# Performance work log

Hardware: AMD Instinct MI355X
Metric: run time of the kernel (lower is better)

The kernel has to match this reference:

```python
import jax, jax.numpy as jnp
import numpy as np
from jax import lax

PRE_NMS_THRESH = 0.05
PRE_NMS_TOP_N = 1000
FINAL_NMS_THRESH = 0.4  # hardcoded in forward(): boxlist_nms(..., 0.4)
MIN_SIZE = 0
STRIDE = 4.0
NEG = -1e9

N, C, H, W = 32, 1, 384, 384


def setup_inputs() -> dict:
    key = jax.random.key(0)
    k1, k2 = jax.random.split(key)
    box_cls = jax.random.uniform(k1, (N, C, H, W), dtype=jnp.float32)
    box_regression = jax.random.normal(k2, (N, 4, H, W), dtype=jnp.float32) * 20.0
    image_sizes = jnp.full((N, 2), H * int(STRIDE), dtype=jnp.int32)
    return {"box_cls": box_cls, "box_regression": box_regression, "image_sizes": image_sizes}


def decode_boxes(quad):
    # quad: [N, 4, H, W]; EAST geometry decode at stride 4 -> xyxy
    n, _, h, w = quad.shape
    x = (jnp.arange(w, dtype=quad.dtype) * STRIDE)[None, :]   # [1, W]
    y = (jnp.arange(h, dtype=quad.dtype) * STRIDE)[:, None]   # [H, 1]
    ymin = y - quad[:, 0]
    xmax = x + quad[:, 1]
    ymax = y + quad[:, 2]
    xmin = x - quad[:, 3]
    return jnp.stack([xmin, ymin, xmax, ymax], axis=1)  # [N, 4, H, W] (permute (3,0,1,2))


def iou_matrix(b):
    # b: [K, 4] xyxy
    x1, y1, x2, y2 = b[:, 0], b[:, 1], b[:, 2], b[:, 3]
    area = jnp.clip(x2 - x1, 0) * jnp.clip(y2 - y1, 0)
    ix1 = jnp.maximum(x1[:, None], x1[None, :])
    iy1 = jnp.maximum(y1[:, None], y1[None, :])
    ix2 = jnp.minimum(x2[:, None], x2[None, :])
    iy2 = jnp.minimum(y2[:, None], y2[None, :])
    inter = jnp.clip(ix2 - ix1, 0) * jnp.clip(iy2 - iy1, 0)
    union = area[:, None] + area[None, :] - inter
    return inter / jnp.maximum(union, 1e-9)


def greedy_nms(boxes, init_keep):
    # boxes: [K, 4] sorted by descending score; init_keep: [K] bool
    K = boxes.shape[0]
    iou = iou_matrix(boxes)
    idx = jnp.arange(K)

    def body(i, keep):
        suppress = (iou[i] > FINAL_NMS_THRESH) & (idx > i)
        return jnp.where(keep[i], keep & ~suppress, keep)

    return lax.fori_loop(0, K, body, init_keep)


def _forward(box_cls, box_regression):
    n, c, h, w = box_cls.shape
    boxes = decode_boxes(box_regression)                       # [N, 4, H, W]
    boxes = boxes.transpose(0, 2, 3, 1).reshape(n, h * w, 4)   # [N, HW, 4]
    scores = box_cls.transpose(0, 2, 3, 1).reshape(n, h * w)   # [N, HW] (C=1)

    # threshold + conditional top-k (padding with NEG emulates variable counts)
    masked = jnp.where(scores > PRE_NMS_THRESH, scores, NEG)
    scores_k, idx_k = lax.top_k(masked, PRE_NMS_TOP_N)         # [N, K], sorted desc
    boxes_k = jnp.take_along_axis(boxes, idx_k[..., None], axis=1)  # [N, K, 4]

    valid = scores_k > PRE_NMS_THRESH
    ws = boxes_k[..., 2] - boxes_k[..., 0]
    hs = boxes_k[..., 3] - boxes_k[..., 1]
    valid = valid & (ws >= MIN_SIZE) & (hs >= MIN_SIZE)        # remove_small_boxes

    keep = jax.vmap(greedy_nms)(boxes_k, valid)                # [N, K]
    out = jnp.concatenate([boxes_k, scores_k[..., None]], axis=-1)
    out = out * keep[..., None].astype(out.dtype)              # [N, K, 5]
    return out, keep


def reference(box_cls, box_regression, image_sizes):
    return _forward(box_cls, box_regression)
```

## Files before the change

kernel.cpp:

```cpp
#include <hip/hip_runtime.h>
#include <stdint.h>

#define NIMG 32
#define WID 384
#define HW 147456
#define TOPK 1000
#define KPAD 1024
#define NBINS 512
#define BIN_SCALEF 512.0f
#define SEGCAP 128
#define CANDCAP 2048
#define THRESH 0.05f
#define PREF_C 0.99f
#define NMS_T 0.4f
#define NBLK 18
#define FINEBINS 256

typedef unsigned long long u64;
typedef unsigned int u32;

#define PIMG_OFF 0
#define PCAND_OFF 4096
#define PBOX_OFF 528384

__device__ __forceinline__ float area_of(float x0, float y0, float x1, float y1) {
  float a = fmaxf(x1 - x0, 0.0f) * fmaxf(y1 - y0, 0.0f);
  asm volatile("" : "+v"(a));
  return a;
}

__device__ __forceinline__ bool iou_gt(float ax0, float ay0, float ax1, float ay1, float aa,
                                       float bx0, float by0, float bx1, float by1, float ba) {
  float ix1 = fmaxf(ax0, bx0);
  float iy1 = fmaxf(ay0, by0);
  float ix2 = fminf(ax1, bx1);
  float iy2 = fminf(ay1, by1);
  float iw = fmaxf(ix2 - ix1, 0.0f);
  float ih = fmaxf(iy2 - iy1, 0.0f);
  float inter = iw * ih;
  asm volatile("" : "+v"(inter));
  float uni = fmaxf(aa + ba - inter, 1e-9f);
  return (inter / uni) > NMS_T;
}

__device__ __forceinline__ u64 shflxor64(u64 v, int m) {
  int lo = __shfl_xor((int)(u32)v, m, 64);
  int hi = __shfl_xor((int)(u32)(v >> 32), m, 64);
  return ((u64)(u32)hi << 32) | (u32)lo;
}

__device__ __forceinline__ u64 make_key(float s, u32 idx) {
  u32 ord = __float_as_uint(s) | 0x80000000u;
  return ((u64)ord << 32) | (u32)(~idx);
}

__device__ __forceinline__ float score_of(u64 key) {
  return __uint_as_float((u32)(key >> 32) & 0x7FFFFFFFu);
}

__device__ __forceinline__ int bin_of(float s) {
  int b = (int)(s * BIN_SCALEF);
  return b < 0 ? 0 : (b > NBINS - 1 ? NBINS - 1 : b);
}

__device__ __forceinline__ int finebin(u64 key) {
  float s = score_of(key);
  int b = (int)((s - 0.99f) * 25600.0f);
  return b < 0 ? 0 : (b > FINEBINS - 1 ? FINEBINS - 1 : b);
}

__global__ __launch_bounds__(256) void scan_kernel(const float* __restrict__ cls,
                                                   const float* __restrict__ reg,
                                                   u32* __restrict__ pimgcnt,
                                                   u64* __restrict__ pcand,
                                                   float4* __restrict__ pbox) {
  __shared__ u64 lbuf[SEGCAP];
  __shared__ u32 lcnt, sbase;
  const int n = blockIdx.y;
  const int tid = threadIdx.x;
  const int lane = tid & 63;
  if (tid == 0) lcnt = 0;
  __syncthreads();

  const float4* src = (const float4*)(cls + (size_t)n * HW) + blockIdx.x * 2048;
  float4 A[8];
#pragma unroll
  for (int v = 0; v < 8; v++) A[v] = src[tid + v * 256];

  const u64 ltmask = (1ull << lane) - 1ull;
#pragma unroll
  for (int v = 0; v < 8; v++) {
    float ss[4] = {A[v].x, A[v].y, A[v].z, A[v].w};
#pragma unroll
    for (int c = 0; c < 4; c++) {
      float s = ss[c];
      bool pc = s > PREF_C;
      u64 m = __ballot(pc);
      if (m) {
        int ldr = __ffsll(m) - 1;
        u32 wb = 0;
        if (lane == ldr) wb = atomicAdd(&lcnt, (u32)__popcll(m));
        wb = (u32)__shfl((int)wb, ldr, 64);
        if (pc) {
          u32 pos = wb + (u32)__popcll(m & ltmask);
          if (pos < SEGCAP) lbuf[pos] = make_key(s, (u32)((blockIdx.x * 2048 + tid + v * 256) * 4 + c));
        }
      }
    }
  }
  __syncthreads();
  const u32 total = lcnt;
  const u32 c = total < SEGCAP ? total : (u32)SEGCAP;
  if (tid == 0) {
    u32 add = (total > SEGCAP) ? (c + 0x100000u) : c;
    sbase = atomicAdd(&pimgcnt[n], add);
  }
  __syncthreads();
  const u32 base = sbase;
  const float* rb = reg + (size_t)n * 4 * HW;
  u64* pk = pcand + (size_t)n * CANDCAP;
  float4* pb = pbox + (size_t)n * CANDCAP;
  for (u32 i = tid; i < c; i += 256) {
    u32 slot = base + i;
    if (slot < CANDCAP) {
      u64 key = lbuf[i];
      u32 idx = ~(u32)(key & 0xFFFFFFFFull);
      int iy = (int)idx / WID;
      int ix = (int)idx - iy * WID;
      float xx = (float)ix * 4.0f;
      float yy = (float)iy * 4.0f;
      float r0 = rb[idx];
      float r1 = rb[HW + idx];
      float r2 = rb[2 * HW + idx];
      float r3 = rb[3 * HW + idx];
      float4 box;
      box.y = yy - r0; box.z = xx + r1; box.w = yy + r2; box.x = xx - r3;
      pk[slot] = key;
      pb[slot] = box;
    }
  }
}

#define REGCHAIN(K, JSTART) do {                                            \
    const bool desc_ = ((tid & ((K) >> 1)) == 0);                           \
    for (int j_ = (JSTART); j_ >= 2; j_ >>= 1) {                            \
      int h_ = j_ >> 1;                                                     \
      bool low_ = (tid & h_) == 0;                                          \
      u64 p0_ = shflxor64(e0, h_), p1_ = shflxor64(e1, h_);                 \
      bool tm_ = (low_ == desc_);                                           \
      e0 = tm_ ? (e0 > p0_ ? e0 : p0_) : (e0 < p0_ ? e0 : p0_);             \
      e1 = tm_ ? (e1 > p1_ ? e1 : p1_) : (e1 < p1_ ? e1 : p1_);             \
    }                                                                       \
    { u64 lo_ = e0 < e1 ? e0 : e1, hi_ = e0 < e1 ? e1 : e0;                 \
      e0 = desc_ ? hi_ : lo_; e1 = desc_ ? lo_ : hi_; }                     \
  } while (0)

__global__ __launch_bounds__(1024) void fused_kernel(const float* __restrict__ cls,
                                                     const float* __restrict__ reg,
                                                     const u32* __restrict__ pimgcnt,
                                                     const u64* __restrict__ pcand,
                                                     const float4* __restrict__ pbox,
                                                     float* __restrict__ out) {
  __shared__ __align__(16) unsigned char smem[90112];
  u64*    CKEY   = (u64*)smem;
  float4* CBOX   = (float4*)(smem + 16384);
  u32*    BINNED = (u32*)(smem + 49152);
  u64*    RKEY   = (u64*)(smem + 57344);
  float4* RBOX   = (float4*)(smem + 65536);
  float* vx    = (float*)smem;
  float* vy    = (float*)(smem + 4096);
  float* vz    = (float*)(smem + 8192);
  float* vw    = (float*)(smem + 12288);
  float* varea = (float*)(smem + 16384);
  u64*   mlds  = (u64*)(smem + 20480);

  __shared__ u32 BINSTART[FINEBINS + 1];
  __shared__ u32 HIST[FINEBINS];
  __shared__ u32 bs[NBINS];
  __shared__ u32 stmp[64];
  __shared__ int stbin;
  __shared__ u32 sflag, sfc;
  __shared__ int sC;
  __shared__ u32 wcnt[16], woff[16];
  __shared__ int pc[136], pk[136];
  __shared__ int sV, snch, snp;
  __shared__ u64 keepsh[16], srem[16];

  const int n = blockIdx.x;
  const int tid = threadIdx.x;
  const int lane = tid & 63;
  const int w = tid >> 6;
  const u64 ltmask = (1ull << lane) - 1ull;

  const u64* gk = pcand + (size_t)n * CANDCAP;
  const float4* gb = pbox + (size_t)n * CANDCAP;
  u64 k0 = gk[tid];
  u64 k1 = gk[tid + 1024];
  float4 b0 = gb[tid];
  float4 b1 = gb[tid + 1024];

  RKEY[tid] = 0ull;
  if (tid < FINEBINS) HIST[tid] = 0;
  if (tid == 0) {
    u32 C = pimgcnt[n];
    sC = (int)C;
    sflag = (C < TOPK || C > CANDCAP) ? 1u : 0u;
    sfc = 0;
  }
  __syncthreads();

  u64 key; float4 b;

  if (sflag == 0) {
    const int C = sC;
    if (tid < C)        { CKEY[tid] = k0;        CBOX[tid] = b0;        atomicAdd(&HIST[finebin(k0)], 1u); }
    if (tid + 1024 < C) { CKEY[tid + 1024] = k1; CBOX[tid + 1024] = b1; atomicAdd(&HIST[finebin(k1)], 1u); }
    __syncthreads();
    if (tid < 64) {
      u32 h0 = HIST[lane * 4 + 0], h1 = HIST[lane * 4 + 1];
      u32 h2 = HIST[lane * 4 + 2], h3 = HIST[lane * 4 + 3];
      u32 t = h0 + h1 + h2 + h3;
      u32 incl = t;
#pragma unroll
      for (int d = 1; d < 64; d <<= 1) {
        u32 v = (u32)__shfl_up((int)incl, d, 64);
        if (lane >= d) incl += v;
      }
      u32 base = incl - t;
      BINSTART[lane * 4 + 0] = base;
      BINSTART[lane * 4 + 1] = base + h0;
      BINSTART[lane * 4 + 2] = base + h0 + h1;
      BINSTART[lane * 4 + 3] = base + h0 + h1 + h2;
      if (lane == 63) BINSTART[FINEBINS] = incl;
      HIST[lane * 4 + 0] = 0; HIST[lane * 4 + 1] = 0;
      HIST[lane * 4 + 2] = 0; HIST[lane * 4 + 3] = 0;
    }
    __syncthreads();
    if (tid < C) {
      int bb = finebin(k0);
      u32 slot = atomicAdd(&HIST[bb], 1u);
      BINNED[BINSTART[bb] + slot] = (u32)tid;
    }
    if (tid + 1024 < C) {
      int bb = finebin(k1);
      u32 slot = atomicAdd(&HIST[bb], 1u);
      BINNED[BINSTART[bb] + slot] = (u32)(tid + 1024);
    }
    __syncthreads();
    if (tid < C) {
      u64 k = k0;
      int bb = finebin(k);
      u32 s0 = BINSTART[bb], s1 = BINSTART[bb + 1];
      u32 g = 0;
      for (u32 j = s0; j < s1; j++) { if (CKEY[BINNED[j]] > k) g++; }
      u32 rank = (u32)C - s1 + g;
      if (rank < KPAD) { RKEY[rank] = k; RBOX[rank] = b0; }
    }
    if (tid + 1024 < C) {
      u64 k = k1;
      int bb = finebin(k);
      u32 s0 = BINSTART[bb], s1 = BINSTART[bb + 1];
      u32 g = 0;
      for (u32 j = s0; j < s1; j++) { if (CKEY[BINNED[j]] > k) g++; }
      u32 rank = (u32)C - s1 + g;
      if (rank < KPAD) { RKEY[rank] = k; RBOX[rank] = b1; }
    }
    __syncthreads();
    key = RKEY[tid];
    b = (key != 0ull) ? RBOX[tid] : make_float4(0.f, 0.f, 0.f, 0.f);
  } else {
    for (int i = tid; i < NBINS; i += 1024) bs[i] = 0;
    CKEY[tid] = 0ull; CKEY[tid + 1024] = 0ull;
    __syncthreads();
    const float* ci = cls + (size_t)n * HW;
    for (int base = 0; base < HW; base += 1024) {
      float s = ci[base + tid];
      if (s > THRESH) atomicAdd(&bs[bin_of(s)], 1u);
    }
    __syncthreads();
    if (tid < 64) {
      u32 cs = 0;
#pragma unroll
      for (int k2 = 0; k2 < 8; k2++) cs += bs[lane * 8 + k2];
      u32 s = cs;
#pragma unroll
      for (int d = 1; d < 64; d <<= 1) {
        u32 v = (u32)__shfl_down((int)s, d, 64);
        if (lane + d < 64) s += v;
      }
      stmp[lane] = s;
      u64 mask = __ballot(s >= TOPK);
      if (lane == 0) {
        int t = 0;
        if (mask) {
          int L = 63 - __clzll(mask);
          u32 acc = (L < 63) ? stmp[L + 1] : 0;
          for (int bb = L * 8 + 7; bb >= L * 8; bb--) {
            acc += bs[bb];
            if (acc >= TOPK) { t = bb; break; }
          }
        }
        stbin = t;
      }
    }
    __syncthreads();
    const int t = stbin;
    for (int base = 0; base < HW; base += 1024) {
      int i = base + tid;
      float s = ci[i];
      bool p = (s > THRESH) && (bin_of(s) >= t);
      u64 m = __ballot(p);
      if (m) {
        int ldr = __ffsll(m) - 1;
        u32 wb = 0;
        if (lane == ldr) wb = atomicAdd(&sfc, (u32)__popcll(m));
        wb = (u32)__shfl((int)wb, ldr, 64);
        if (p) { u32 pos = wb + (u32)__popcll(m & ltmask); if (pos < CANDCAP) CKEY[pos] = make_key(s, (u32)i); }
      }
    }
    __syncthreads();
    {
      u64 e0 = CKEY[2 * tid], e1 = CKEY[2 * tid + 1];
      REGCHAIN(2, 1); REGCHAIN(4, 2); REGCHAIN(8, 4); REGCHAIN(16, 8);
      REGCHAIN(32, 16); REGCHAIN(64, 32); REGCHAIN(128, 64);
      for (int k = 256; k <= CANDCAP; k <<= 1) {
        CKEY[2 * tid] = e0; CKEY[2 * tid + 1] = e1;
        __syncthreads();
        for (int j = k >> 1; j >= 128; j >>= 1) {
          int i = ((tid & ~(j - 1)) << 1) | (tid & (j - 1));
          u64 a = CKEY[i], bb = CKEY[i + j];
          bool desc = ((i & k) == 0);
          if (desc ? (a < bb) : (a > bb)) { CKEY[i] = bb; CKEY[i + j] = a; }
          __syncthreads();
        }
        e0 = CKEY[2 * tid]; e1 = CKEY[2 * tid + 1];
        REGCHAIN(k, 64);
      }
      CKEY[2 * tid] = e0; CKEY[2 * tid + 1] = e1;
      __syncthreads();
    }
    key = CKEY[tid];
    b = make_float4(0.f, 0.f, 0.f, 0.f);
    if (key != 0ull && tid < TOPK) {
      u32 idx = ~(u32)(key & 0xFFFFFFFFull);
      int iy = (int)idx / WID;
      int ix = (int)idx - iy * WID;
      float xx = (float)ix * 4.0f;
      float yy = (float)iy * 4.0f;
      const float* rb = reg + (size_t)n * 4 * HW;
      float r0 = rb[idx];
      float r1 = rb[HW + idx];
      float r2 = rb[2 * HW + idx];
      float r3 = rb[3 * HW + idx];
      b.y = yy - r0; b.z = xx + r1; b.w = yy + r2; b.x = xx - r3;
    }
  }
  float s = score_of(key);
  __syncthreads();

  bool vb = (tid < TOPK) && (s > THRESH) && (b.z - b.x >= 0.0f) && (b.w - b.y >= 0.0f);
  vx[tid] = 0.0f; vy[tid] = 0.0f; vz[tid] = 0.0f; vw[tid] = 0.0f;
  varea[tid] = 0.0f;
  u64 vm = __ballot(vb);
  if (lane == 0) wcnt[w] = (u32)__popcll(vm);
  if (tid < 16) { srem[tid] = 0ull; keepsh[tid] = 0ull; }
  __syncthreads();
  if (tid < 64) {
    u32 v = (lane < 16) ? wcnt[lane] : 0u;
    u32 incl = v;
#pragma unroll
    for (int d = 1; d < 16; d <<= 1) {
      u32 t = (u32)__shfl_up((int)incl, d, 64);
      if (lane >= d) incl += t;
    }
    if (lane < 16) woff[lane] = incl - v;
    if (lane == 15) {
      int V = (int)incl;
      int nch = (V + 63) >> 6;
      sV = V; snch = nch; snp = nch * (nch + 1) / 2;
    }
  }
  __syncthreads();
  const int V = sV, nch = snch, npairs = snp;

  int pos = -1;
  if (vb) {
    pos = (int)(woff[w] + (u32)__popcll(vm & ltmask));
    vx[pos] = b.x; vy[pos] = b.y; vz[pos] = b.z; vw[pos] = b.w;
    varea[pos] = area_of(b.x, b.y, b.z, b.w);
  }
  if (tid < npairs) {
    int p = tid, c = 0, base = 0;
    while (p >= base + (nch - c)) { base += nch - c; c++; }
    pc[tid] = c; pk[tid] = c + (p - base);
  }
  __syncthreads();

  {
    int prevc = -1;
    float cx0 = 0.f, cy0 = 0.f, cx1 = 0.f, cy1 = 0.f, ca = 0.f;
    for (int r = w; r < npairs * 64; r += 16) {
      int p = r >> 6, i = r & 63;
      int c = pc[p], k = pk[p];
      if (c != prevc) {
        int ci = c * 64 + lane;
        cx0 = vx[ci]; cy0 = vy[ci]; cx1 = vz[ci]; cy1 = vw[ci]; ca = varea[ci];
        prevc = c;
      }
      int ri = k * 64 + i;
      float rx0 = vx[ri], ry0 = vy[ri], rx1 = vz[ri], ry1 = vw[ri], ra = varea[ri];
      bool pred = iou_gt(rx0, ry0, rx1, ry1, ra, cx0, cy0, cx1, cy1, ca);
      u64 m = __ballot(pred);
      if (lane == 0) mlds[r] = m;
    }
  }
  __syncthreads();

  if (tid < 64) {
    for (int c = 0; c < nch; c++) {
      int pbase = c * nch - (c * (c - 1)) / 2 - c;
      u64 diag = mlds[(pbase + c) * 64 + lane];
      u64 ainit = (V >= (c + 1) * 64) ? ~0ull
                : ((V > c * 64) ? ((1ull << (V - c * 64)) - 1ull) : 0ull);
      u64 alive;
      {
        u64 a = ainit & ~srem[c];
        u32 alo2 = __builtin_amdgcn_readfirstlane((u32)a);
        u32 ahi2 = __builtin_amdgcn_readfirstlane((u32)(a >> 32));
        alive = ((u64)ahi2 << 32) | alo2;
      }
      u32 rlo = (u32)diag, rhi = (u32)(diag >> 32);
      u64 cur = alive;
      while (cur) {
        int i = __ffsll(cur) - 1;
        u32 rl = __builtin_amdgcn_readlane(rlo, i);
        u32 rh = __builtin_amdgcn_readlane(rhi, i);
        u64 rowi = ((u64)rh << 32) | rl;
        u64 lowmask = (i == 63) ? ~0ull : ((1ull << (i + 1)) - 1ull);
        rowi &= ~lowmask;
        alive &= ~rowi;
        cur &= ~rowi;
        cur &= cur - 1;
      }
      if (lane == 0) keepsh[c] = alive;
      const u64 K = alive;
      for (int k = c + 1; k < nch; k++) {
        bool sup = (mlds[(pbase + k) * 64 + lane] & K) != 0ull;
        u64 mres = __ballot(sup);
        if (lane == 0) srem[k] |= mres;
      }
    }
  }
  __syncthreads();

  u64 kb = (vb && pos >= 0) ? ((keepsh[pos >> 6] >> (pos & 63)) & 1ull) : 0ull;
  if (tid < TOPK) {
    float f = (float)kb;
    size_t ob = (size_t)n * (TOPK * 5) + (size_t)tid * 5;
    out[ob + 0] = kb ? b.x : 0.0f;
    out[ob + 1] = kb ? b.y : 0.0f;
    out[ob + 2] = kb ? b.z : 0.0f;
    out[ob + 3] = kb ? b.w : 0.0f;
    out[ob + 4] = kb ? s : 0.0f;
    out[(size_t)NIMG * TOPK * 5 + (size_t)n * TOPK + tid] = f;
  }
}

extern "C" void kernel_launch(void* const* d_in, const int* in_sizes, int n_in,
                              void* d_out, int out_size, void* d_ws, size_t ws_size,
                              hipStream_t stream) {
  const float* cls = (const float*)d_in[0];
  const float* reg = (const float*)d_in[1];
  float* out = (float*)d_out;

  uint8_t* ws = (uint8_t*)d_ws;
  u32* pimgcnt = (u32*)(ws + PIMG_OFF);
  u64* pcand = (u64*)(ws + PCAND_OFF);
  float4* pbox = (float4*)(ws + PBOX_OFF);

  hipMemsetAsync(pimgcnt, 0, NIMG * sizeof(u32), stream);
  scan_kernel<<<dim3(NBLK, NIMG), 256, 0, stream>>>(cls, reg, pimgcnt, pcand, pbox);
  fused_kernel<<<NIMG, 1024, 0, stream>>>(cls, reg, pimgcnt, pcand, pbox, out);
}
```

Before: 157.1 us.

## Replace global atomic compaction with per-segment candidate slots and in-kernel prefix

Each scan block now writes its candidates into a fixed per-segment region and records its own count, instead of reserving space through a global atomic counter per image. The fused kernel computes a prefix sum over the 18 segment counts with wave shuffles and compacts the candidates into shared memory. This removes the hipMemsetAsync launch and the global atomic serialization, at the cost of reading 2304 slots per image instead of 2048. The shared CBOX staging buffer is also dropped, since boxes now stay in registers.

```diff
diff --git a/kernel.cpp b/kernel.cpp
--- a/kernel.cpp
+++ b/kernel.cpp
@@ -9,6 +9,7 @@
 #define NBINS 512
 #define BIN_SCALEF 512.0f
 #define SEGCAP 128
+#define NSLOT (NBLK * SEGCAP)
 #define CANDCAP 2048
 #define THRESH 0.05f
 #define PREF_C 0.99f
@@ -19,9 +20,9 @@
 typedef unsigned long long u64;
 typedef unsigned int u32;
 
-#define PIMG_OFF 0
+#define PCNT_OFF 0
 #define PCAND_OFF 4096
-#define PBOX_OFF 528384
+#define PBOX_OFF  593920
 
 __device__ __forceinline__ float area_of(float x0, float y0, float x1, float y1) {
   float a = fmaxf(x1 - x0, 0.0f) * fmaxf(y1 - y0, 0.0f);
@@ -71,11 +72,11 @@
 
 __global__ __launch_bounds__(256) void scan_kernel(const float* __restrict__ cls,
                                                    const float* __restrict__ reg,
-                                                   u32* __restrict__ pimgcnt,
+                                                   u32* __restrict__ pcnt,
                                                    u64* __restrict__ pcand,
                                                    float4* __restrict__ pbox) {
   __shared__ u64 lbuf[SEGCAP];
-  __shared__ u32 lcnt, sbase;
+  __shared__ u32 lcnt;
   const int n = blockIdx.y;
   const int tid = threadIdx.x;
   const int lane = tid & 63;
@@ -109,35 +110,27 @@
     }
   }
   __syncthreads();
-  const u32 total = lcnt;
-  const u32 c = total < SEGCAP ? total : (u32)SEGCAP;
-  if (tid == 0) {
-    u32 add = (total > SEGCAP) ? (c + 0x100000u) : c;
-    sbase = atomicAdd(&pimgcnt[n], add);
-  }
-  __syncthreads();
-  const u32 base = sbase;
+  const int seg = n * NBLK + blockIdx.x;
+  if (tid == 0) pcnt[seg] = (lcnt > SEGCAP) ? 0xFFFFFFFFu : lcnt;
+  u32 c = lcnt < SEGCAP ? lcnt : (u32)SEGCAP;
   const float* rb = reg + (size_t)n * 4 * HW;
-  u64* pk = pcand + (size_t)n * CANDCAP;
-  float4* pb = pbox + (size_t)n * CANDCAP;
+  u64* pk = pcand + (size_t)seg * SEGCAP;
+  float4* pb = pbox + (size_t)seg * SEGCAP;
   for (u32 i = tid; i < c; i += 256) {
-    u32 slot = base + i;
-    if (slot < CANDCAP) {
-      u64 key = lbuf[i];
-      u32 idx = ~(u32)(key & 0xFFFFFFFFull);
-      int iy = (int)idx / WID;
-      int ix = (int)idx - iy * WID;
-      float xx = (float)ix * 4.0f;
-      float yy = (float)iy * 4.0f;
-      float r0 = rb[idx];
-      float r1 = rb[HW + idx];
-      float r2 = rb[2 * HW + idx];
-      float r3 = rb[3 * HW + idx];
-      float4 box;
-      box.y = yy - r0; box.z = xx + r1; box.w = yy + r2; box.x = xx - r3;
-      pk[slot] = key;
-      pb[slot] = box;
-    }
+    u64 key = lbuf[i];
+    u32 idx = ~(u32)(key & 0xFFFFFFFFull);
+    int iy = (int)idx / WID;
+    int ix = (int)idx - iy * WID;
+    float xx = (float)ix * 4.0f;
+    float yy = (float)iy * 4.0f;
+    float r0 = rb[idx];
+    float r1 = rb[HW + idx];
+    float r2 = rb[2 * HW + idx];
+    float r3 = rb[3 * HW + idx];
+    float4 box;
+    box.y = yy - r0; box.z = xx + r1; box.w = yy + r2; box.x = xx - r3;
+    pk[i] = key;
+    pb[i] = box;
   }
 }
 
@@ -157,16 +150,15 @@
 
 __global__ __launch_bounds__(1024) void fused_kernel(const float* __restrict__ cls,
                                                      const float* __restrict__ reg,
-                                                     const u32* __restrict__ pimgcnt,
+                                                     const u32* __restrict__ pcnt,
                                                      const u64* __restrict__ pcand,
                                                      const float4* __restrict__ pbox,
                                                      float* __restrict__ out) {
   __shared__ __align__(16) unsigned char smem[90112];
   u64*    CKEY   = (u64*)smem;
-  float4* CBOX   = (float4*)(smem + 16384);
-  u32*    BINNED = (u32*)(smem + 49152);
-  u64*    RKEY   = (u64*)(smem + 57344);
-  float4* RBOX   = (float4*)(smem + 65536);
+  u32*    BINNED = (u32*)(smem + 16384);
+  u64*    RKEY   = (u64*)(smem + 24576);
+  float4* RBOX   = (float4*)(smem + 32768);
   float* vx    = (float*)smem;
   float* vy    = (float*)(smem + 4096);
   float* vz    = (float*)(smem + 8192);
@@ -176,6 +168,8 @@
 
   __shared__ u32 BINSTART[FINEBINS + 1];
   __shared__ u32 HIST[FINEBINS];
+  __shared__ u32 scnt[NBLK];
+  __shared__ u32 soff[NBLK];
   __shared__ u32 bs[NBINS];
   __shared__ u32 stmp[64];
   __shared__ int stbin;
@@ -192,29 +186,57 @@
   const int w = tid >> 6;
   const u64 ltmask = (1ull << lane) - 1ull;
 
-  const u64* gk = pcand + (size_t)n * CANDCAP;
-  const float4* gb = pbox + (size_t)n * CANDCAP;
+  const u64* gk = pcand + (size_t)n * NSLOT;
+  const float4* gb = pbox + (size_t)n * NSLOT;
   u64 k0 = gk[tid];
   u64 k1 = gk[tid + 1024];
   float4 b0 = gb[tid];
   float4 b1 = gb[tid + 1024];
-
+  u64 k2 = 0; float4 b2 = make_float4(0.f, 0.f, 0.f, 0.f);
+  if (tid < NSLOT - 2048) { k2 = gk[tid + 2048]; b2 = gb[tid + 2048]; }
+
+  if (tid < 64) {
+    u32 cnt = 0; bool ovf = false;
+    if (lane < NBLK) {
+      cnt = pcnt[n * NBLK + lane];
+      if (cnt == 0xFFFFFFFFu) { ovf = true; cnt = 0; }
+    }
+    u32 incl = cnt;
+#pragma unroll
+    for (int d = 1; d < 32; d <<= 1) {
+      u32 v = (u32)__shfl_up((int)incl, d, 64);
+      if (lane >= d) incl += v;
+    }
+    if (lane < NBLK) { scnt[lane] = cnt; soff[lane] = incl - cnt; }
+    u64 om = __ballot(ovf);
+    if (lane == NBLK - 1) {
+      u32 C = incl;
+      sC = (int)C;
+      sflag = (om != 0ull || C < TOPK || C > CANDCAP) ? 1u : 0u;
+      sfc = 0;
+    }
+  }
   RKEY[tid] = 0ull;
   if (tid < FINEBINS) HIST[tid] = 0;
-  if (tid == 0) {
-    u32 C = pimgcnt[n];
-    sC = (int)C;
-    sflag = (C < TOPK || C > CANDCAP) ? 1u : 0u;
-    sfc = 0;
-  }
   __syncthreads();
 
   u64 key; float4 b;
 
   if (sflag == 0) {
     const int C = sC;
-    if (tid < C)        { CKEY[tid] = k0;        CBOX[tid] = b0;        atomicAdd(&HIST[finebin(k0)], 1u); }
-    if (tid + 1024 < C) { CKEY[tid + 1024] = k1; CBOX[tid + 1024] = b1; atomicAdd(&HIST[finebin(k1)], 1u); }
+    u32 o0 = 0, o1 = 0, o2 = 0; bool v0 = false, v1 = false, v2 = false;
+    {
+      int seg = tid >> 7, i = tid & 127;
+      if ((u32)i < scnt[seg]) { v0 = true; o0 = soff[seg] + (u32)i; CKEY[o0] = k0; atomicAdd(&HIST[finebin(k0)], 1u); }
+    }
+    {
+      int slot = tid + 1024; int seg = slot >> 7, i = slot & 127;
+      if ((u32)i < scnt[seg]) { v1 = true; o1 = soff[seg] + (u32)i; CKEY[o1] = k1; atomicAdd(&HIST[finebin(k1)], 1u); }
+    }
+    if (tid < NSLOT - 2048) {
+      int slot = tid + 2048; int seg = slot >> 7, i = slot & 127;
+      if ((u32)i < scnt[seg]) { v2 = true; o2 = soff[seg] + (u32)i; CKEY[o2] = k2; atomicAdd(&HIST[finebin(k2)], 1u); }
+    }
     __syncthreads();
     if (tid < 64) {
       u32 h0 = HIST[lane * 4 + 0], h1 = HIST[lane * 4 + 1];
@@ -236,34 +258,30 @@
       HIST[lane * 4 + 2] = 0; HIST[lane * 4 + 3] = 0;
     }
     __syncthreads();
-    if (tid < C) {
+    if (v0) { int bb = finebin(k0); u32 sl = atomicAdd(&HIST[bb], 1u); BINNED[BINSTART[bb] + sl] = o0; }
+    if (v1) { int bb = finebin(k1); u32 sl = atomicAdd(&HIST[bb], 1u); BINNED[BINSTART[bb] + sl] = o1; }
+    if (v2) { int bb = finebin(k2); u32 sl = atomicAdd(&HIST[bb], 1u); BINNED[BINSTART[bb] + sl] = o2; }
+    __syncthreads();
+    if (v0) {
       int bb = finebin(k0);
-      u32 slot = atomicAdd(&HIST[bb], 1u);
-      BINNED[BINSTART[bb] + slot] = (u32)tid;
-    }
-    if (tid + 1024 < C) {
+      u32 s0 = BINSTART[bb], s1 = BINSTART[bb + 1], g = 0;
+      for (u32 j = s0; j < s1; j++) { if (CKEY[BINNED[j]] > k0) g++; }
+      u32 rank = (u32)C - s1 + g;
+      if (rank < KPAD) { RKEY[rank] = k0; RBOX[rank] = b0; }
+    }
+    if (v1) {
       int bb = finebin(k1);
-      u32 slot = atomicAdd(&HIST[bb], 1u);
-      BINNED[BINSTART[bb] + slot] = (u32)(tid + 1024);
-    }
-    __syncthreads();
-    if (tid < C) {
-      u64 k = k0;
-      int bb = finebin(k);
-      u32 s0 = BINSTART[bb], s1 = BINSTART[bb + 1];
-      u32 g = 0;
-      for (u32 j = s0; j < s1; j++) { if (CKEY[BINNED[j]] > k) g++; }
+      u32 s0 = BINSTART[bb], s1 = BINSTART[bb + 1], g = 0;
+      for (u32 j = s0; j < s1; j++) { if (CKEY[BINNED[j]] > k1) g++; }
       u32 rank = (u32)C - s1 + g;
-      if (rank < KPAD) { RKEY[rank] = k; RBOX[rank] = b0; }
-    }
-    if (tid + 1024 < C) {
-      u64 k = k1;
-      int bb = finebin(k);
-      u32 s0 = BINSTART[bb], s1 = BINSTART[bb + 1];
-      u32 g = 0;
-      for (u32 j = s0; j < s1; j++) { if (CKEY[BINNED[j]] > k) g++; }
+      if (rank < KPAD) { RKEY[rank] = k1; RBOX[rank] = b1; }
+    }
+    if (v2) {
+      int bb = finebin(k2);
+      u32 s0 = BINSTART[bb], s1 = BINSTART[bb + 1], g = 0;
+      for (u32 j = s0; j < s1; j++) { if (CKEY[BINNED[j]] > k2) g++; }
       u32 rank = (u32)C - s1 + g;
-      if (rank < KPAD) { RKEY[rank] = k; RBOX[rank] = b1; }
+      if (rank < KPAD) { RKEY[rank] = k2; RBOX[rank] = b2; }
     }
     __syncthreads();
     key = RKEY[tid];
@@ -281,7 +299,7 @@
     if (tid < 64) {
       u32 cs = 0;
 #pragma unroll
-      for (int k2 = 0; k2 < 8; k2++) cs += bs[lane * 8 + k2];
+      for (int k2i = 0; k2i < 8; k2i++) cs += bs[lane * 8 + k2i];
       u32 s = cs;
 #pragma unroll
       for (int d = 1; d < 64; d <<= 1) {
@@ -474,11 +492,10 @@
   float* out = (float*)d_out;
 
   uint8_t* ws = (uint8_t*)d_ws;
-  u32* pimgcnt = (u32*)(ws + PIMG_OFF);
+  u32* pcnt = (u32*)(ws + PCNT_OFF);
   u64* pcand = (u64*)(ws + PCAND_OFF);
   float4* pbox = (float4*)(ws + PBOX_OFF);
 
-  hipMemsetAsync(pimgcnt, 0, NIMG * sizeof(u32), stream);
-  scan_kernel<<<dim3(NBLK, NIMG), 256, 0, stream>>>(cls, reg, pimgcnt, pcand, pbox);
-  fused_kernel<<<NIMG, 1024, 0, stream>>>(cls, reg, pimgcnt, pcand, pbox, out);
-}
+  scan_kernel<<<dim3(NBLK, NIMG), 256, 0, stream>>>(cls, reg, pcnt, pcand, pbox);
+  fused_kernel<<<NIMG, 1024, 0, stream>>>(cls, reg, pcnt, pcand, pbox, out);
+}
```

Measured after the change: 153.5 us. -2.3%, faster.
